# Kernel optimization log

Hardware: AMD Instinct MI355X
Metric: run time of the kernel (lower is better)

Reference implementation:

```python
import jax, jax.numpy as jnp
import numpy as np

HIDDEN = 2048
NUM_HEADS = 16
HEAD_DIM = 128
WINDOW_SIZE = 512
NUM_GLOBAL = 16
SCALING = HEAD_DIM ** -0.5


def setup_inputs() -> dict:
    key = jax.random.key(0)
    ks = jax.random.split(key, 5)
    std = HIDDEN ** -0.5
    hidden_states = jax.random.normal(ks[0], (1, 4096, HIDDEN), dtype=jnp.float32)
    # Linear weights stored as (in, out) so y = x @ W
    Wq = jax.random.normal(ks[1], (HIDDEN, NUM_HEADS * HEAD_DIM), dtype=jnp.float32) * std
    Wk = jax.random.normal(ks[2], (HIDDEN, NUM_HEADS * HEAD_DIM), dtype=jnp.float32) * std
    Wv = jax.random.normal(ks[3], (HIDDEN, NUM_HEADS * HEAD_DIM), dtype=jnp.float32) * std
    Wo = jax.random.normal(ks[4], (NUM_HEADS * HEAD_DIM, HIDDEN), dtype=jnp.float32) * std
    return {"hidden_states": hidden_states, "Wq": Wq, "Wk": Wk, "Wv": Wv, "Wo": Wo}


def _sliding_mask(q_len: int, kv_len: int) -> jnp.ndarray:
    q_pos = jnp.arange(q_len)[:, None]
    kv_pos = jnp.arange(kv_len)[None, :]
    half_window = WINDOW_SIZE // 2
    local = jnp.abs(q_pos - kv_pos) < half_window
    glob = (q_pos < NUM_GLOBAL) | (kv_pos < NUM_GLOBAL)
    mask = local | glob
    return jnp.where(mask, 0.0, -jnp.inf).astype(jnp.float32)


def reference(hidden_states, Wq, Wk, Wv, Wo):
    bsz, q_len, _ = hidden_states.shape
    q = (hidden_states @ Wq).reshape(bsz, q_len, NUM_HEADS, HEAD_DIM).transpose(0, 2, 1, 3)
    k = (hidden_states @ Wk).reshape(bsz, q_len, NUM_HEADS, HEAD_DIM).transpose(0, 2, 1, 3)
    v = (hidden_states @ Wv).reshape(bsz, q_len, NUM_HEADS, HEAD_DIM).transpose(0, 2, 1, 3)
    mask = _sliding_mask(q_len, q_len)[None, None]  # [1,1,S,S]
    scores = jnp.einsum("bhqd,bhkd->bhqk", q, k) * SCALING + mask
    attn = jax.nn.softmax(scores.astype(jnp.float32), axis=-1).astype(q.dtype)
    out = jnp.einsum("bhqk,bhkd->bhqd", attn, v)
    out = out.transpose(0, 2, 1, 3).reshape(bsz, q_len, NUM_HEADS * HEAD_DIM)
    return out @ Wo
```

## Files before the change

kernel.cpp:

```cpp
#include <hip/hip_runtime.h>
#include <stdint.h>

#define SEQ    4096
#define HID    2048
#define NQKV   6144
#define QKW    4096
#define NH     16
#define HD     128
#define SCALE  0.08838834764831845f
#define GQC    32

typedef unsigned short u16;
typedef __attribute__((ext_vector_type(8))) short bf16x8;
typedef __attribute__((ext_vector_type(4))) float f32x4;

__device__ __forceinline__ u16 f2bf(float f) {
  union { float f; unsigned u; } v; v.f = f;
  unsigned r = v.u + 0x7FFFu + ((v.u >> 16) & 1u);
  return (u16)(r >> 16);
}

__device__ __forceinline__ float bf2f(u16 b) {
  union { unsigned u; float f; } c; c.u = ((unsigned)b) << 16; return c.f;
}

__device__ __forceinline__ void async16(const u16* g, u16* l) {
  __builtin_amdgcn_global_load_lds(
      (const __attribute__((address_space(1))) unsigned int*)g,
      (__attribute__((address_space(3))) unsigned int*)l, 16, 0, 0);
}

__global__ __launch_bounds__(256) void prep(const float* __restrict__ X,
                                            const float* __restrict__ W0,
                                            const float* __restrict__ W1,
                                            const float* __restrict__ W2,
                                            const float* __restrict__ W3,
                                            u16* __restrict__ Xbf,
                                            u16* __restrict__ Wcat,
                                            u16* __restrict__ Wot,
                                            unsigned* __restrict__ cnt) {
  const int bx = blockIdx.x;
  const int t = threadIdx.x;
  if (bx == 0 && t < NH) cnt[t] = 0u;
  if (bx < 8192) {
    int i = bx * 256 + t;
    float4 v = ((const float4*)X)[i];
    ushort4 o;
    o.x = f2bf(v.x); o.y = f2bf(v.y); o.z = f2bf(v.z); o.w = f2bf(v.w);
    ((ushort4*)Xbf)[i] = o;
    return;
  }
  __shared__ __align__(16) u16 Ts[64 * 68];
  const int b = bx - 8192;
  const int z = b >> 10;
  const int k0 = ((b >> 5) & 31) * 64;
  const int n0 = (b & 31) * 64;
  const float* W = (z == 0) ? W0 : (z == 1) ? W1 : (z == 2) ? W2 : W3;
  u16* Wt = (z < 3) ? (Wcat + (size_t)z * 2048 * 2048) : Wot;
#pragma unroll
  for (int p = 0; p < 4; ++p) {
    int f = (t + p * 256) * 4;
    int r = f >> 6, c = f & 63;
    float4 v = *(const float4*)&W[(size_t)(k0 + r) * 2048 + n0 + c];
    ushort4 o; o.x = f2bf(v.x); o.y = f2bf(v.y); o.z = f2bf(v.z); o.w = f2bf(v.w);
    *(ushort4*)&Ts[r * 68 + c] = o;
  }
  __syncthreads();
#pragma unroll
  for (int p = 0; p < 4; ++p) {
    int g = (t + p * 256) * 4;
    int r = g >> 6, c = g & 63;
    ushort4 o;
    o.x = Ts[(c + 0) * 68 + r];
    o.y = Ts[(c + 1) * 68 + r];
    o.z = Ts[(c + 2) * 68 + r];
    o.w = Ts[(c + 3) * 68 + r];
    *(ushort4*)&Wt[(size_t)(n0 + r) * 2048 + k0 + c] = o;
  }
}

template <typename OutT, bool WVT>
__global__ __launch_bounds__(256) void gemm_bt(const u16* __restrict__ A,
                                               const u16* __restrict__ B,
                                               OutT* __restrict__ C,
                                               u16* __restrict__ VTout,
                                               int K, int ldc) {
  __shared__ __align__(16) u16 As0[128 * 32];
  __shared__ __align__(16) u16 As1[128 * 32];
  __shared__ __align__(16) u16 Bs0[128 * 32];
  __shared__ __align__(16) u16 Bs1[128 * 32];
  const int m0 = blockIdx.y * 128;
  const int n0 = blockIdx.x * 128;
  const int tid = threadIdx.x;
  const int wid = tid >> 6;
  const int lane = tid & 63;
  const int wm = wid & 1, wn = wid >> 1;
  const int l15 = lane & 15, g4 = lane >> 4;

  const int srow = wid * 32 + (lane >> 2);
  const int scol = (lane & 3) * 8;

  f32x4 acc[4][4] = {};

  const u16* pa0 = &A[(size_t)(m0 + srow) * K + scol];
  const u16* pa1 = &A[(size_t)(m0 + srow + 16) * K + scol];
  const u16* pb0 = &B[(size_t)(n0 + srow) * K + scol];
  const u16* pb1 = &B[(size_t)(n0 + srow + 16) * K + scol];
  const int lo0 = (wid * 32) * 32, lo1 = (wid * 32 + 16) * 32;

  for (int kt = 0; kt < K; kt += 64) {
    __syncthreads();
    async16(pa0 + kt, &As0[lo0]);
    async16(pa1 + kt, &As0[lo1]);
    async16(pb0 + kt, &Bs0[lo0]);
    async16(pb1 + kt, &Bs0[lo1]);
    async16(pa0 + kt + 32, &As1[lo0]);
    async16(pa1 + kt + 32, &As1[lo1]);
    async16(pb0 + kt + 32, &Bs1[lo0]);
    async16(pb1 + kt + 32, &Bs1[lo1]);
    __syncthreads();
    {
      bf16x8 af[4], bfr[4];
#pragma unroll
      for (int i = 0; i < 4; ++i)
        af[i] = *(const bf16x8*)&As0[(wm * 64 + i * 16 + l15) * 32 + g4 * 8];
#pragma unroll
      for (int i = 0; i < 4; ++i)
        bfr[i] = *(const bf16x8*)&Bs0[(wn * 64 + i * 16 + l15) * 32 + g4 * 8];
#pragma unroll
      for (int mi = 0; mi < 4; ++mi)
#pragma unroll
        for (int ni = 0; ni < 4; ++ni)
          acc[mi][ni] = __builtin_amdgcn_mfma_f32_16x16x32_bf16(af[mi], bfr[ni], acc[mi][ni], 0, 0, 0);
    }
    {
      bf16x8 af[4], bfr[4];
#pragma unroll
      for (int i = 0; i < 4; ++i)
        af[i] = *(const bf16x8*)&As1[(wm * 64 + i * 16 + l15) * 32 + g4 * 8];
#pragma unroll
      for (int i = 0; i < 4; ++i)
        bfr[i] = *(const bf16x8*)&Bs1[(wn * 64 + i * 16 + l15) * 32 + g4 * 8];
#pragma unroll
      for (int mi = 0; mi < 4; ++mi)
#pragma unroll
        for (int ni = 0; ni < 4; ++ni)
          acc[mi][ni] = __builtin_amdgcn_mfma_f32_16x16x32_bf16(af[mi], bfr[ni], acc[mi][ni], 0, 0, 0);
    }
  }

  if (WVT && n0 >= QKW) {
#pragma unroll
    for (int mi = 0; mi < 4; ++mi)
#pragma unroll
      for (int ni = 0; ni < 4; ++ni) {
        const int nv = n0 - QKW + wn * 64 + ni * 16 + l15;
        const int hh = nv >> 7, dd = nv & 127;
        u16* base = &VTout[((size_t)hh * HD + dd) * SEQ];
        const int mb = m0 + wm * 64 + mi * 16 + g4 * 4;
        u16 pk[4];
#pragma unroll
        for (int r = 0; r < 4; ++r) pk[r] = f2bf(acc[mi][ni][r]);
        *(uint2*)&base[mb] = *(uint2*)pk;
      }
  } else {
#pragma unroll
    for (int mi = 0; mi < 4; ++mi)
#pragma unroll
      for (int ni = 0; ni < 4; ++ni) {
        const int n = n0 + wn * 64 + ni * 16 + l15;
#pragma unroll
        for (int r = 0; r < 4; ++r) {
          const int m = m0 + wm * 64 + mi * 16 + g4 * 4 + r;
          float v = acc[mi][ni][r];
          if constexpr (sizeof(OutT) == 2) {
            C[(size_t)m * ldc + n] = (OutT)f2bf(v);
          } else {
            C[(size_t)m * ldc + n] = v;
          }
        }
      }
  }
}

__global__ __launch_bounds__(256, 2) void attn_fused(const u16* __restrict__ qk,
                                                     const u16* __restrict__ vt,
                                                     u16* __restrict__ out,
                                                     float* __restrict__ Opart,
                                                     float* __restrict__ MLpart,
                                                     unsigned* __restrict__ cnt) {
  __shared__ __align__(16) u16 smem[24576];
  __shared__ unsigned lastflag;
  const int h = blockIdx.y;
  const int tid = threadIdx.x;
  const int lane = tid & 63;

  if (blockIdx.x < 32) {
    u16* Ks  = smem;
    u16* VTs = smem + 8192;
    u16* Ps  = smem + 16384;
    const int q0 = blockIdx.x * 128;
    const int w = tid >> 6;
    const int l15 = lane & 15, g4 = lane >> 4, l7 = lane & 7;

    bf16x8 qf[2][4];
#pragma unroll
    for (int qs = 0; qs < 2; ++qs) {
      const u16* qrow = &qk[(size_t)(q0 + w * 32 + qs * 16 + l15) * QKW + h * HD + g4 * 8];
#pragma unroll
      for (int kk = 0; kk < 4; ++kk) qf[qs][kk] = *(const bf16x8*)&qrow[kk * 32];
    }

    float m_run[2] = {-1e30f, -1e30f}, l_run[2] = {0.f, 0.f};
    f32x4 o[2][8] = {};

    int lo = q0 - 255;
    int lo_blk = (lo < 0) ? 0 : (lo >> 6);
    int hi_blk = (q0 + 382) >> 6;
    if (hi_blk > 63) hi_blk = 63;
    const int extra = (lo_blk > 0) ? 1 : 0;
    const int nsteps = hi_blk - lo_blk + 1 + extra;

    for (int step = 0; step < nsteps; ++step) {
      const int kb = (extra && step == 0) ? 0 : (lo_blk + step - extra);
      const int kv0 = kb * 64;
      __syncthreads();
#pragma unroll
      for (int p = 0; p < 4; ++p) {
        const int r = w * 16 + p * 4 + (lane >> 4);
        const u16* src = &qk[(size_t)(kv0 + r) * QKW + 2048 + h * HD + (((lane & 15) ^ (r & 15)) * 8)];
        async16(src, &Ks[(w * 16 + p * 4) * 128]);
      }
#pragma unroll
      for (int p = 0; p < 4; ++p) {
        const int r = w * 32 + p * 8 + (lane >> 3);
        const u16* src = &vt[(size_t)h * (HD * SEQ) + (size_t)r * SEQ + kv0 + (((lane & 7) ^ (r & 7)) * 8)];
        async16(src, &VTs[(w * 32 + p * 8) * 64]);
      }
      __syncthreads();

      f32x4 st[2][4] = {};
#pragma unroll
      for (int kk = 0; kk < 4; ++kk) {
        bf16x8 ak[4];
#pragma unroll
        for (int t4 = 0; t4 < 4; ++t4)
          ak[t4] = *(const bf16x8*)&Ks[(t4 * 16 + l15) * 128 + (((kk * 4 + g4) ^ l15) * 8)];
#pragma unroll
        for (int qs = 0; qs < 2; ++qs)
#pragma unroll
          for (int t4 = 0; t4 < 4; ++t4)
            st[qs][t4] = __builtin_amdgcn_mfma_f32_16x16x32_bf16(ak[t4], qf[qs][kk], st[qs][t4], 0, 0, 0);
      }

#pragma unroll
      for (int qs = 0; qs < 2; ++qs) {
        const int q = q0 + w * 32 + qs * 16 + l15;
        float cmax = -1e30f;
#pragma unroll
        for (int t4 = 0; t4 < 4; ++t4)
#pragma unroll
          for (int r = 0; r < 4; ++r) {
            int kv = kv0 + t4 * 16 + g4 * 4 + r;
            int dq = q - kv; if (dq < 0) dq = -dq;
            bool ok = (dq < 256) || (kv < 16);
            float s = ok ? st[qs][t4][r] * SCALE : -1e30f;
            st[qs][t4][r] = s;
            cmax = fmaxf(cmax, s);
          }
        cmax = fmaxf(cmax, __shfl_xor(cmax, 16, 64));
        cmax = fmaxf(cmax, __shfl_xor(cmax, 32, 64));
        float mnew = fmaxf(m_run[qs], cmax);
        float csum = 0.f;
#pragma unroll
        for (int t4 = 0; t4 < 4; ++t4)
#pragma unroll
          for (int r = 0; r < 4; ++r) {
            float p = __expf(st[qs][t4][r] - mnew);
            st[qs][t4][r] = p;
            csum += p;
          }
        csum += __shfl_xor(csum, 16, 64);
        csum += __shfl_xor(csum, 32, 64);
        float a = __expf(m_run[qs] - mnew);
        m_run[qs] = mnew;
        l_run[qs] = l_run[qs] * a + csum;

#pragma unroll
        for (int t4 = 0; t4 < 4; ++t4) {
          u16 pk[4];
#pragma unroll
          for (int r = 0; r < 4; ++r) pk[r] = f2bf(st[qs][t4][r]);
          int c8 = t4 * 2 + (g4 >> 1);
          *(uint2*)&Ps[(w * 32 + qs * 16 + l15) * 64 + ((c8 ^ l7) * 8) + (g4 & 1) * 4] = *(uint2*)pk;
        }
#pragma unroll
        for (int nt = 0; nt < 8; ++nt)
#pragma unroll
          for (int r = 0; r < 4; ++r) o[qs][nt][r] *= a;
      }

#pragma unroll
      for (int ks = 0; ks < 2; ++ks) {
        bf16x8 ap[2];
#pragma unroll
        for (int qs = 0; qs < 2; ++qs)
          ap[qs] = *(const bf16x8*)&Ps[(w * 32 + qs * 16 + l15) * 64 + (((ks * 4 + g4) ^ l7) * 8)];
#pragma unroll
        for (int nt = 0; nt < 8; ++nt) {
          bf16x8 bv = *(const bf16x8*)&VTs[(nt * 16 + l15) * 64 + (((ks * 4 + g4) ^ l7) * 8)];
#pragma unroll
          for (int qs = 0; qs < 2; ++qs)
            o[qs][nt] = __builtin_amdgcn_mfma_f32_16x16x32_bf16(bv, ap[qs], o[qs][nt], 0, 0, 0);
        }
      }
    }

#pragma unroll
    for (int qs = 0; qs < 2; ++qs) {
      if (q0 + w * 32 + qs * 16 < 16) continue;
      const int q = q0 + w * 32 + qs * 16 + l15;
      const float inv = 1.f / l_run[qs];
#pragma unroll
      for (int nt = 0; nt < 8; ++nt) {
        u16 pk[4];
#pragma unroll
        for (int r = 0; r < 4; ++r) pk[r] = f2bf(o[qs][nt][r] * inv);
        *(uint2*)&out[(size_t)q * HID + h * HD + nt * 16 + g4 * 4] = *(uint2*)pk;
      }
    }
    return;
  }

  {
    u16* Ks = smem;
    u16* Vs = smem + 8704;
    const int chunk = blockIdx.x - 32;
    const int t = tid;
    const int q = t >> 4, dg = t & 15;

    float qr[8];
    {
      bf16x8 v = *(const bf16x8*)&qk[(size_t)q * QKW + h * HD + dg * 8];
#pragma unroll
      for (int j = 0; j < 8; ++j) qr[j] = bf2f((u16)v[j]);
    }
    float m_run = -1e30f, l_run = 0.f, o[8] = {};
    const int kvbase = chunk * (SEQ / GQC);

    for (int st = 0; st < (SEQ / GQC) / 64; ++st) {
      const int kv0 = kvbase + st * 64;
      __syncthreads();
#pragma unroll
      for (int p = 0; p < 4; ++p) {
        int f = (t + p * 256) * 8;
        int r = f >> 7, c = f & 127;
        *(uint4*)&Ks[r * 136 + c] = *(const uint4*)&qk[(size_t)(kv0 + r) * QKW + 2048 + h * HD + c];
      }
#pragma unroll
      for (int p = 0; p < 4; ++p) {
        int id = p * 256 + t;
        int d = id >> 3, c8 = id & 7;
        uint4 v = *(const uint4*)&vt[(size_t)h * (HD * SEQ) + (size_t)d * SEQ + kv0 + c8 * 8];
        const u16* pv16 = (const u16*)&v;
#pragma unroll
        for (int j = 0; j < 8; ++j) Vs[(c8 * 8 + j) * 136 + d] = pv16[j];
      }
      __syncthreads();
      for (int kv = 0; kv < 64; ++kv) {
        bf16x8 kr = *(const bf16x8*)&Ks[kv * 136 + dg * 8];
        float s = 0.f;
#pragma unroll
        for (int j = 0; j < 8; ++j) s += qr[j] * bf2f((u16)kr[j]);
        s += __shfl_xor(s, 1, 64); s += __shfl_xor(s, 2, 64);
        s += __shfl_xor(s, 4, 64); s += __shfl_xor(s, 8, 64);
        s *= SCALE;
        float mnew = fmaxf(m_run, s);
        float alpha = __expf(m_run - mnew);
        float p = __expf(s - mnew);
        m_run = mnew;
        l_run = l_run * alpha + p;
        bf16x8 vr = *(const bf16x8*)&Vs[kv * 136 + dg * 8];
#pragma unroll
        for (int j = 0; j < 8; ++j) o[j] = o[j] * alpha + p * bf2f((u16)vr[j]);
      }
    }
    float* op = &Opart[(((size_t)h * GQC + chunk) * 16 + q) * HD + dg * 8];
#pragma unroll
    for (int j = 0; j < 8; ++j) op[j] = o[j];
    if (dg == 0) {
      float* ml = &MLpart[(((size_t)h * GQC + chunk) * 16 + q) * 2];
      ml[0] = m_run; ml[1] = l_run;
    }

    __syncthreads();
    if (t == 0) {
      __threadfence();
      lastflag = (atomicAdd(&cnt[h], 1u) == GQC - 1) ? 1u : 0u;
    }
    __syncthreads();
    if (lastflag) {
      __threadfence();
      float M = -1e30f;
      for (int c = 0; c < GQC; ++c)
        M = fmaxf(M, MLpart[(((size_t)h * GQC + c) * 16 + q) * 2]);
      float L = 0.f, oo[8] = {};
      for (int c = 0; c < GQC; ++c) {
        const float* ml = &MLpart[(((size_t)h * GQC + c) * 16 + q) * 2];
        float e = __expf(ml[0] - M);
        L += e * ml[1];
        const float* opc = &Opart[(((size_t)h * GQC + c) * 16 + q) * HD + dg * 8];
#pragma unroll
        for (int j = 0; j < 8; ++j) oo[j] += e * opc[j];
      }
      float inv = 1.f / L;
      u16 tmp[8];
#pragma unroll
      for (int j = 0; j < 8; ++j) tmp[j] = f2bf(oo[j] * inv);
      *(uint4*)&out[(size_t)q * HID + h * HD + dg * 8] = *(uint4*)tmp;
    }
  }
}

extern "C" void kernel_launch(void* const* d_in, const int* in_sizes, int n_in,
                              void* d_out, int out_size, void* d_ws, size_t ws_size,
                              hipStream_t stream) {
  const float* X  = (const float*)d_in[0];
  const float* Wq = (const float*)d_in[1];
  const float* Wk = (const float*)d_in[2];
  const float* Wv = (const float*)d_in[3];
  const float* Wo = (const float*)d_in[4];
  float* out = (float*)d_out;

  char* ws = (char*)d_ws;
  u16* Xbf    = (u16*)(ws);
  u16* Wcat   = (u16*)(ws + (size_t)(16 << 20));
  u16* AttnO  = (u16*)(ws + (size_t)(16 << 20));
  float* Opart  = (float*)(ws + (size_t)(32 << 20));
  float* MLpart = (float*)(ws + (size_t)(36 << 20));
  unsigned* cnt = (unsigned*)d_out;
  u16* QK     = (u16*)(ws + (size_t)(40 << 20));
  u16* VT     = (u16*)(ws + (size_t)(72 << 20));
  u16* Wot    = (u16*)(ws + (size_t)(88 << 20));

  prep<<<dim3(12288), 256, 0, stream>>>(X, Wq, Wk, Wv, Wo, Xbf, Wcat, Wot, cnt);
  gemm_bt<u16, true><<<dim3(48, 32), 256, 0, stream>>>(Xbf, Wcat, QK, VT, HID, QKW);
  attn_fused<<<dim3(32 + GQC, NH), 256, 0, stream>>>(QK, VT, AttnO, Opart, MLpart, cnt);
  gemm_bt<float, false><<<dim3(16, 32), 256, 0, stream>>>(AttnO, Wot, out, nullptr, HID, HID);
}
```

Baseline: 414.4 us.

## Replace QKV projection GEMM with 256x256-tile, 8-wave pipelined kernel

Adds a new GEMM kernel that computes 256x256 output tiles per block with 512 threads. The tile is split into quadrants processed in eight phases, each overlapping async global-to-LDS staging of the next K-slice with MFMA work, using barriers and setprio interleaving. The QKV projection launch switches to this kernel (24x16 grid instead of 48x32). The aim is more data reuse per loaded byte and better latency hiding, at the cost of fewer blocks (384), which may underfill the GPU, and heavier register and LDS use.

```diff
diff --git a/kernel.cpp b/kernel.cpp
--- a/kernel.cpp
+++ b/kernel.cpp
@@ -183,6 +183,153 @@
   }
 }
 
+template <int QM, int QN, bool VM4, typename StageFn>
+__device__ __forceinline__ void phase8(const u16* __restrict__ ah,
+                                       const u16* __restrict__ bh,
+                                       f32x4 (&acc)[2][2][4][2],
+                                       int aoff0, int boff0, int c0, int c1,
+                                       StageFn&& stg) {
+  bf16x8 af[4][2], bv[2][2];
+#pragma unroll
+  for (int fm = 0; fm < 4; ++fm) {
+    af[fm][0] = *(const bf16x8*)&ah[aoff0 + fm * 1024 + c0];
+    af[fm][1] = *(const bf16x8*)&ah[aoff0 + fm * 1024 + c1];
+  }
+#pragma unroll
+  for (int fn = 0; fn < 2; ++fn) {
+    bv[fn][0] = *(const bf16x8*)&bh[boff0 + fn * 1024 + c0];
+    bv[fn][1] = *(const bf16x8*)&bh[boff0 + fn * 1024 + c1];
+  }
+  stg();
+  asm volatile("" ::: "memory");
+  __builtin_amdgcn_s_barrier();
+  asm volatile("s_waitcnt lgkmcnt(0)" ::: "memory");
+  __builtin_amdgcn_sched_barrier(0);
+  __builtin_amdgcn_s_setprio(1);
+#pragma unroll
+  for (int fm = 0; fm < 4; ++fm)
+#pragma unroll
+    for (int fn = 0; fn < 2; ++fn) {
+      acc[QM][QN][fm][fn] = __builtin_amdgcn_mfma_f32_16x16x32_bf16(af[fm][0], bv[fn][0], acc[QM][QN][fm][fn], 0, 0, 0);
+      acc[QM][QN][fm][fn] = __builtin_amdgcn_mfma_f32_16x16x32_bf16(af[fm][1], bv[fn][1], acc[QM][QN][fm][fn], 0, 0, 0);
+    }
+  __builtin_amdgcn_s_setprio(0);
+  if constexpr (VM4) asm volatile("s_waitcnt vmcnt(4)" ::: "memory");
+  asm volatile("" ::: "memory");
+  __builtin_amdgcn_s_barrier();
+}
+
+template <typename OutT, bool WVT>
+__global__ __launch_bounds__(512, 2) void gemm256(const u16* __restrict__ A,
+                                                  const u16* __restrict__ B,
+                                                  OutT* __restrict__ C,
+                                                  u16* __restrict__ VTout,
+                                                  int K, int ldc) {
+  __shared__ __align__(16) u16 As[2][2][128 * 64];
+  __shared__ __align__(16) u16 Bs[2][2][128 * 64];
+  const int m0 = blockIdx.y * 256;
+  const int n0 = blockIdx.x * 256;
+  const int tid = threadIdx.x;
+  const int lane = tid & 63;
+  const int wid = tid >> 6;
+  const int wm = wid >> 2, wn = wid & 3;
+  const int l15 = lane & 15, g4 = lane >> 4;
+
+  const int r0 = tid >> 3;
+  const int csw = ((tid & 7) ^ (r0 & 7)) * 8;
+  const u16* Ag = A + (size_t)(m0 + r0) * K + csw;
+  const u16* Bg = B + (size_t)(n0 + r0) * K + csw;
+
+  const int aoff0 = (wm * 64 + l15) * 64;
+  const int boff0 = (wn * 32 + l15) * 64;
+  const int c0 = ((g4 ^ (l15 & 7)) << 3);
+  const int c1 = (((4 + g4) ^ (l15 & 7)) << 3);
+
+  auto stage = [&](const u16* src, int half, int tile, u16* dst) {
+    const u16* s = src + (size_t)half * 128 * K + (size_t)tile * 64;
+    u16* d = dst + wid * 512;
+    async16(s, d);
+    async16(s + (size_t)64 * K, d + 4096);
+  };
+
+  f32x4 acc[2][2][4][2] = {};
+
+  stage(Ag, 0, 0, &As[0][0][0]);
+  stage(Bg, 0, 0, &Bs[0][0][0]);
+  stage(Ag, 1, 0, &As[0][1][0]);
+  stage(Bg, 1, 0, &Bs[0][1][0]);
+  stage(Ag, 0, 1, &As[1][0][0]);
+  stage(Bg, 0, 1, &Bs[1][0][0]);
+  asm volatile("s_waitcnt vmcnt(4)" ::: "memory");
+  asm volatile("" ::: "memory");
+  __builtin_amdgcn_s_barrier();
+
+  const int NT = K >> 6;
+  for (int it = 0; it < (NT >> 1); ++it) {
+    const int tA = 2 * it + 1;
+    const int tB = (2 * it + 2) & (NT - 1);
+    const int tC = (2 * it + 3) & (NT - 1);
+    phase8<0, 0, false>(&As[0][0][0], &Bs[0][0][0], acc, aoff0, boff0, c0, c1,
+                        [&] { stage(Ag, 1, tA, &As[1][1][0]); });
+    phase8<0, 1, false>(&As[0][0][0], &Bs[0][1][0], acc, aoff0, boff0, c0, c1,
+                        [&] { stage(Bg, 1, tA, &Bs[1][1][0]); });
+    phase8<1, 0, false>(&As[0][1][0], &Bs[0][0][0], acc, aoff0, boff0, c0, c1,
+                        [&] { stage(Ag, 0, tB, &As[0][0][0]); });
+    phase8<1, 1, true>(&As[0][1][0], &Bs[0][1][0], acc, aoff0, boff0, c0, c1,
+                       [&] { stage(Bg, 0, tB, &Bs[0][0][0]); });
+    phase8<0, 0, false>(&As[1][0][0], &Bs[1][0][0], acc, aoff0, boff0, c0, c1,
+                        [&] { stage(Ag, 1, tB, &As[0][1][0]); });
+    phase8<0, 1, false>(&As[1][0][0], &Bs[1][1][0], acc, aoff0, boff0, c0, c1,
+                        [&] { stage(Bg, 1, tB, &Bs[0][1][0]); });
+    phase8<1, 0, false>(&As[1][1][0], &Bs[1][0][0], acc, aoff0, boff0, c0, c1,
+                        [&] { stage(Ag, 0, tC, &As[1][0][0]); });
+    phase8<1, 1, true>(&As[1][1][0], &Bs[1][1][0], acc, aoff0, boff0, c0, c1,
+                       [&] { stage(Bg, 0, tC, &Bs[1][0][0]); });
+  }
+  asm volatile("s_waitcnt vmcnt(0)" ::: "memory");
+
+  if (WVT && n0 >= QKW) {
+#pragma unroll
+    for (int qm = 0; qm < 2; ++qm)
+#pragma unroll
+      for (int qn = 0; qn < 2; ++qn)
+#pragma unroll
+        for (int fm = 0; fm < 4; ++fm)
+#pragma unroll
+          for (int fn = 0; fn < 2; ++fn) {
+            const int nv = n0 - QKW + qn * 128 + wn * 32 + fn * 16 + l15;
+            const int hh = nv >> 7, dd = nv & 127;
+            u16* base = &VTout[((size_t)hh * HD + dd) * SEQ];
+            const int mb = m0 + qm * 128 + wm * 64 + fm * 16 + g4 * 4;
+            u16 pk[4];
+#pragma unroll
+            for (int r = 0; r < 4; ++r) pk[r] = f2bf(acc[qm][qn][fm][fn][r]);
+            *(uint2*)&base[mb] = *(uint2*)pk;
+          }
+  } else {
+#pragma unroll
+    for (int qm = 0; qm < 2; ++qm)
+#pragma unroll
+      for (int qn = 0; qn < 2; ++qn)
+#pragma unroll
+        for (int fm = 0; fm < 4; ++fm)
+#pragma unroll
+          for (int fn = 0; fn < 2; ++fn) {
+            const int n = n0 + qn * 128 + wn * 32 + fn * 16 + l15;
+#pragma unroll
+            for (int r = 0; r < 4; ++r) {
+              const int m = m0 + qm * 128 + wm * 64 + fm * 16 + g4 * 4 + r;
+              float v = acc[qm][qn][fm][fn][r];
+              if constexpr (sizeof(OutT) == 2) {
+                C[(size_t)m * ldc + n] = (OutT)f2bf(v);
+              } else {
+                C[(size_t)m * ldc + n] = v;
+              }
+            }
+          }
+  }
+}
+
 __global__ __launch_bounds__(256, 2) void attn_fused(const u16* __restrict__ qk,
                                                      const u16* __restrict__ vt,
                                                      u16* __restrict__ out,
@@ -444,7 +591,7 @@
   u16* Wot    = (u16*)(ws + (size_t)(88 << 20));
 
   prep<<<dim3(12288), 256, 0, stream>>>(X, Wq, Wk, Wv, Wo, Xbf, Wcat, Wot, cnt);
-  gemm_bt<u16, true><<<dim3(48, 32), 256, 0, stream>>>(Xbf, Wcat, QK, VT, HID, QKW);
+  gemm256<u16, true><<<dim3(24, 16), 512, 0, stream>>>(Xbf, Wcat, QK, VT, HID, QKW);
   attn_fused<<<dim3(32 + GQC, NH), 256, 0, stream>>>(QK, VT, AttnO, Opart, MLpart, cnt);
   gemm_bt<float, false><<<dim3(16, 32), 256, 0, stream>>>(AttnO, Wot, out, nullptr, HID, HID);
 }
```

New measurement: 435.5 us. 1.05x slower.
